# Kernel optimization log

Hardware: AMD Instinct MI355X
Metric: run time of the kernel (lower is better)

Reference implementation:

```python
import jax, jax.numpy as jnp
import numpy as np

EPS = 1e-7
MIN_NORM = 1e-15
PROJ_EPS = 1e-5
NEG_SLOPE = 0.2
HEADS = 4


def artanh(x):
    return jnp.arctanh(jnp.clip(x, -1.0 + EPS, 1.0 - EPS))


def _norm(x):
    return jnp.clip(jnp.linalg.norm(x, axis=-1, keepdims=True), MIN_NORM)


def proj(x):
    # project onto Poincare ball (c=1)
    n = _norm(x)
    maxn = 1.0 - PROJ_EPS
    return jnp.where(n > maxn, x / n * maxn, x)


def expmap0(u):
    n = _norm(u)
    return jnp.tanh(n) * u / n


def logmap0(x):
    n = _norm(x)
    return artanh(n) * x / n


def mobius_add(x, y):
    x2 = jnp.sum(x * x, axis=-1, keepdims=True)
    y2 = jnp.sum(y * y, axis=-1, keepdims=True)
    xy = jnp.sum(x * y, axis=-1, keepdims=True)
    num = (1.0 + 2.0 * xy + y2) * x + (1.0 - x2) * y
    den = 1.0 + 2.0 * xy + x2 * y2
    return num / jnp.clip(den, MIN_NORM)


def pdist(x, y):
    # Poincare distance, c=1 -> [...,] scalar
    ma = mobius_add(-x, y)
    return 2.0 * artanh(jnp.linalg.norm(ma, axis=-1))


def mobius_scalar_mul(r, x):
    n = _norm(x)
    return jnp.tanh(r * artanh(n)) * x / n


def mobius_matvec(W, x):
    # x: [N,din], W: [dout,din]
    mx = x @ W.T
    n_x = _norm(x)
    n_mx = _norm(mx)
    return jnp.tanh(n_mx / n_x * artanh(n_x)) * mx / n_mx


def segment_softmax(logits, seg, num_segments):
    m = jax.ops.segment_max(logits, seg, num_segments=num_segments)
    m = jnp.where(jnp.isfinite(m), m, 0.0)
    e = jnp.exp(logits - m[seg])
    s = jax.ops.segment_sum(e, seg, num_segments=num_segments)
    return e / (s[seg] + 1e-16)


def setup_inputs() -> dict:
    N, E, D = 50000, 500000, 128
    H = HEADS
    Dh = D // H
    ks = jax.random.split(jax.random.key(0), 12)
    # edges without self-loops (reference re-adds them, mirroring remove/add_self_loops)
    src = jax.random.randint(ks[0], (E,), 0, N)
    off = jax.random.randint(ks[1], (E,), 1, N)
    dst = (src + off) % N
    edge_index = jnp.stack([src, dst]).astype(jnp.int32)
    x_e = 0.1 * jax.random.normal(ks[2], (N, D), dtype=jnp.float32)
    x_h = proj(expmap0(0.05 * jax.random.normal(ks[3], (N, D), dtype=jnp.float32)))
    sc = 1.0 / np.sqrt(D)
    W_e = sc * jax.random.normal(ks[4], (D, D), dtype=jnp.float32)
    b_lin_e = jnp.zeros((D,), jnp.float32)
    att_e = 0.1 * jax.random.normal(ks[5], (1, H, 2 * Dh), dtype=jnp.float32)
    b_e = jnp.zeros((D,), jnp.float32)
    W_h = sc * jax.random.normal(ks[6], (D, D), dtype=jnp.float32)
    b_lin_h = jnp.zeros((D,), jnp.float32)
    att_h = 0.1 * jax.random.normal(ks[7], (1, H, 2 * Dh), dtype=jnp.float32)
    b_h = jnp.zeros((D,), jnp.float32)
    att_hf = 0.1 * jax.random.normal(ks[8], (1, 1), dtype=jnp.float32)
    att_ef = 0.1 * jax.random.normal(ks[9], (1, 1), dtype=jnp.float32)
    return {"x_e": x_e, "x_h": x_h, "edge_index": edge_index,
            "W_e": W_e, "b_lin_e": b_lin_e, "att_e": att_e, "b_e": b_e,
            "W_h": W_h, "b_lin_h": b_lin_h, "att_h": att_h, "b_h": b_h,
            "att_hf": att_hf, "att_ef": att_ef}


def reference(x_e, x_h, edge_index, W_e, b_lin_e, att_e, b_e,
              W_h, b_lin_h, att_h, b_h, att_hf, att_ef):
    N, D = x_e.shape
    H = HEADS
    Dh = att_e.shape[-1] // 2
    loop = jnp.arange(N, dtype=edge_index.dtype)
    src = jnp.concatenate([edge_index[0], loop])  # j (source)
    dst = jnp.concatenate([edge_index[1], loop])  # i (target, softmax segment)

    # ---- Euclidean GAT branch (GATConv) ----
    xe = (x_e @ W_e.T + b_lin_e).reshape(N, H, Dh)
    a_i = jnp.sum(xe * att_e[:, :, :Dh], axis=-1)  # [N,H] target part
    a_j = jnp.sum(xe * att_e[:, :, Dh:], axis=-1)  # [N,H] source part
    alpha = jax.nn.leaky_relu(a_i[dst] + a_j[src], NEG_SLOPE)  # [E',H]
    alpha = segment_softmax(alpha, dst, N)
    agg = jax.ops.segment_sum(xe[src] * alpha[:, :, None], dst, num_segments=N)
    e_out = jax.nn.relu(agg.reshape(N, H * Dh) + b_e)

    # ---- Hyperbolic GAT branch (HGATConv with HypLinear) ----
    mv = proj(mobius_matvec(W_h, x_h))
    hb = proj(expmap0(b_lin_h))  # proj_tan0 is identity on Poincare ball
    xh = proj(mobius_add(mv, hb))  # [N,D] hyperbolic points (original_x)
    lx = logmap0(xh).reshape(N, H, Dh)
    hi = jnp.sum(lx * att_h[:, :, :Dh], axis=-1)
    hj = jnp.sum(lx * att_h[:, :, Dh:], axis=-1)
    alpha_h = hi[dst] + hj[src]  # [E',H]
    d = pdist(xh[dst], xh[src])  # [E'] hyperbolic edge distances
    d = segment_softmax(d, dst, N)[:, None]
    alpha_h = jax.nn.leaky_relu(alpha_h * d, NEG_SLOPE)
    alpha_h = segment_softmax(alpha_h, dst, N)
    agg_h = jax.ops.segment_sum(lx[src] * alpha_h[:, :, None], dst, num_segments=N)
    out_t = jax.nn.relu(agg_h.reshape(N, H * Dh) + b_h)  # tangent at origin
    h_out = proj(expmap0(out_t))

    # ---- HFusion: fuse Euclidean into hyperbolic ----
    ye = proj(expmap0(e_out))
    dist_f = (pdist(h_out, ye) * att_hf[0, 0])[:, None]  # [N,1]
    xe2 = proj(mobius_scalar_mul(dist_f, ye))
    h_fused = proj(mobius_add(h_out, xe2))

    # ---- EFusion: fuse hyperbolic into Euclidean ----
    lh = logmap0(h_out)
    de = (jnp.sum((lh - e_out) ** 2, axis=-1) * att_ef[0, 0])[:, None]
    e_fused = e_out + de * lh

    return jnp.stack([h_fused, e_fused])  # [2,N,D]
```

## Files before the change

### kernel.cpp

```cpp
#include <hip/hip_runtime.h>
#include <hip/hip_fp16.h>
#include <math.h>

typedef _Float16 h2 __attribute__((ext_vector_type(2)));
typedef _Float16 h8 __attribute__((ext_vector_type(8)));
typedef float f32x4 __attribute__((ext_vector_type(4)));

#define MAXN_BALL (1.0f - 1e-5f)
#define ART_CLIP  (1.0f - 1e-7f)
#define MAXD 48
#define SROW 64

__device__ __forceinline__ float f_rcp(float x)  { return __builtin_amdgcn_rcpf(x); }
__device__ __forceinline__ float f_exp(float x)  { return __expf(x); }
__device__ __forceinline__ float f_log(float x)  { return __logf(x); }
__device__ __forceinline__ float f_tanh(float x) {
    float ax = fabsf(x);
    float e = __expf(2.f * ax);
    float t = 1.f - 2.f * f_rcp(e + 1.f);
    return copysignf(t, x);
}
__device__ __forceinline__ float f_atanh(float x) {
    x = fminf(x, ART_CLIP);
    return 0.5f * f_log((1.f + x) * f_rcp(1.f - x));
}
__device__ __forceinline__ float leaky(float x) { return x > 0.0f ? x : 0.2f * x; }

union F4H8 { float4 f; h2 h[4]; };
union F2H4 { float2 f; h2 h[2]; };
union H8U  { h8 v; h2 h[4]; };
union H8F  { float4 f; h8 v; h2 h[4]; };

__device__ __forceinline__ h2 pk16(float x, float y) {
    union { decltype(__builtin_amdgcn_cvt_pkrtz(0.f, 0.f)) a; h2 b; } u;
    u.a = __builtin_amdgcn_cvt_pkrtz(x, y);
    return u.b;
}

__global__ __launch_bounds__(256) void k_wcvt(const float* __restrict__ W0,
                                              const float* __restrict__ W1,
                                              h2* __restrict__ W16,
                                              int* __restrict__ slots,
                                              int N, int cblocks) {
    int b = blockIdx.x, t = threadIdx.x;
    if (b < cblocks) {
        int zi = b * 256 + t;
        if (zi < N) slots[zi * SROW] = 0;
        return;
    }
    int tw = (b - cblocks) * 256 + t;
    const float* W = (tw < 2048) ? W0 : W1;
    int c = (tw & 2047) * 8;
    float4 a = *(const float4*)(W + c);
    float4 bb = *(const float4*)(W + c + 4);
    F4H8 u;
    u.h[0] = pk16(a.x, a.y);  u.h[1] = pk16(a.z, a.w);
    u.h[2] = pk16(bb.x, bb.y); u.h[3] = pk16(bb.z, bb.w);
    *(float4*)&W16[(tw >> 11) * 8192 + (c >> 1)] = u.f;
}

__global__ __launch_bounds__(256) void k_prep_fused(
        const float* __restrict__ x_e, const float* __restrict__ x_h,
        const h2* __restrict__ W16,
        const float* __restrict__ b_lin_e, const float* __restrict__ b_lin_h,
        const float* __restrict__ att_e, const float* __restrict__ att_h,
        h2* __restrict__ xe16, h2* __restrict__ xh16,
        float* __restrict__ aux_j, float* __restrict__ aux_i,
        const int* __restrict__ ei, int* __restrict__ slots,
        int N, int E) {
    int t = threadIdx.x;
    if (blockIdx.y == 1) {
        int idx = blockIdx.x * 256 + t;
        if (idx < E + N) {
            int s, d;
            if (idx < E) { s = ei[idx]; d = ei[E + idx]; } else { s = d = idx - E; }
            int p = atomicAdd(&slots[d * SROW], 1);
            if (p < MAXD) slots[d * SROW + 1 + p] = s;
        }
        return;
    }
    int wv = t >> 6, l = t & 63;
    int rt = blockIdx.x * 4 + wv;
    if (rt * 16 >= N) return;
    int lane16 = l & 15, quad = l >> 4;
    int r = rt * 16 + lane16;
    int rr = (r < N) ? r : (N - 1);

    const float* Xrow = &x_e[(size_t)rr * 128 + quad * 8];
    H8U bfr[4];
#pragma unroll
    for (int ks = 0; ks < 4; ++ks) {
        float4 xa = *(const float4*)(Xrow + ks * 32);
        float4 xb = *(const float4*)(Xrow + ks * 32 + 4);
        bfr[ks].h[0] = pk16(xa.x, xa.y); bfr[ks].h[1] = pk16(xa.z, xa.w);
        bfr[ks].h[2] = pk16(xb.x, xb.y); bfr[ks].h[3] = pk16(xb.z, xb.w);
    }
    float pi[4] = {0.f, 0.f, 0.f, 0.f}, pj[4] = {0.f, 0.f, 0.f, 0.f};
#pragma unroll
    for (int ct = 0; ct < 8; ++ct) {
        const h2* Wrow = &W16[(ct * 16 + lane16) * 64 + quad * 4];
        f32x4 acc = {0.f, 0.f, 0.f, 0.f};
#pragma unroll
        for (int ks = 0; ks < 4; ++ks) {
            H8F a;
            a.f = *(const float4*)(Wrow + ks * 16);
            acc = __builtin_amdgcn_mfma_f32_16x16x32_f16(a.v, bfr[ks].v, acc, 0, 0, 0);
        }
        int obase = ct * 16 + quad * 4;
        float4 bb = *(const float4*)&b_lin_e[obase];
        F2H4 u;
        u.h[0] = pk16(acc[0] + bb.x, acc[1] + bb.y);
        u.h[1] = pk16(acc[2] + bb.z, acc[3] + bb.w);
        if (r < N) *(float2*)&xe16[(size_t)r * 64 + (obase >> 1)] = u.f;
        float4 xe4 = make_float4((float)u.h[0].x, (float)u.h[0].y,
                                 (float)u.h[1].x, (float)u.h[1].y);
        int hd = ct >> 1, w0 = (ct & 1) * 16 + quad * 4;
        float4 aT = *(const float4*)&att_e[hd * 64 + w0];
        float4 aS = *(const float4*)&att_e[hd * 64 + 32 + w0];
        pi[hd] += xe4.x * aT.x + xe4.y * aT.y + xe4.z * aT.z + xe4.w * aT.w;
        pj[hd] += xe4.x * aS.x + xe4.y * aS.y + xe4.z * aS.z + xe4.w * aS.w;
    }

    const float* Xrow1 = &x_h[(size_t)rr * 128 + quad * 8];
    float nx2 = 0.f;
#pragma unroll
    for (int ks = 0; ks < 4; ++ks) {
        float4 xa = *(const float4*)(Xrow1 + ks * 32);
        float4 xb = *(const float4*)(Xrow1 + ks * 32 + 4);
        nx2 += xa.x * xa.x + xa.y * xa.y + xa.z * xa.z + xa.w * xa.w
             + xb.x * xb.x + xb.y * xb.y + xb.z * xb.z + xb.w * xb.w;
        bfr[ks].h[0] = pk16(xa.x, xa.y); bfr[ks].h[1] = pk16(xa.z, xa.w);
        bfr[ks].h[2] = pk16(xb.x, xb.y); bfr[ks].h[3] = pk16(xb.z, xb.w);
    }
    f32x4 mx[8];
    float4 bh[8];
    float nmx2 = 0.f, dmb = 0.f, nb2 = 0.f;
#pragma unroll
    for (int ct = 0; ct < 8; ++ct) {
        const h2* Wrow = &W16[8192 + (ct * 16 + lane16) * 64 + quad * 4];
        f32x4 acc = {0.f, 0.f, 0.f, 0.f};
#pragma unroll
        for (int ks = 0; ks < 4; ++ks) {
            H8F a;
            a.f = *(const float4*)(Wrow + ks * 16);
            acc = __builtin_amdgcn_mfma_f32_16x16x32_f16(a.v, bfr[ks].v, acc, 0, 0, 0);
        }
        mx[ct] = acc;
        int obase = ct * 16 + quad * 4;
        float4 bv = *(const float4*)&b_lin_h[obase];
        bh[ct] = bv;
        nmx2 += acc[0] * acc[0] + acc[1] * acc[1] + acc[2] * acc[2] + acc[3] * acc[3];
        dmb  += acc[0] * bv.x + acc[1] * bv.y + acc[2] * bv.z + acc[3] * bv.w;
        nb2  += bv.x * bv.x + bv.y * bv.y + bv.z * bv.z + bv.w * bv.w;
    }
#pragma unroll
    for (int m = 16; m <= 32; m <<= 1) {
        nx2 += __shfl_xor(nx2, m, 64); nmx2 += __shfl_xor(nmx2, m, 64);
        dmb += __shfl_xor(dmb, m, 64); nb2  += __shfl_xor(nb2, m, 64);
    }

    float nxr = sqrtf(nx2),  nxc = fmaxf(nxr, 1e-15f);
    float nmxr = sqrtf(nmx2), nmxc = fmaxf(nmxr, 1e-15f);
    float tt = f_tanh(nmxc * f_rcp(nxc) * f_atanh(nxc));
    float c_m = tt * f_rcp(nmxc);
    float nmv = tt * (nmxr * f_rcp(nmxc));
    if (nmv > MAXN_BALL) { c_m *= MAXN_BALL / nmv; nmv = MAXN_BALL; }

    float nbr = sqrtf(nb2), nbc = fmaxf(nbr, 1e-15f);
    float tb = f_tanh(nbc);
    float c_b = tb * f_rcp(nbc);
    float nhb = tb * (nbr * f_rcp(nbc));
    if (nhb > MAXN_BALL) { c_b *= MAXN_BALL / nhb; nhb = MAXN_BALL; }

    float xy = c_m * c_b * dmb;
    float x2 = nmv * nmv, y2 = nhb * nhb;
    float den = fmaxf(1.f + 2.f * xy + x2 * y2, 1e-15f);
    float rden = f_rcp(den);
    float al = (1.f + 2.f * xy + y2) * c_m * rden;
    float be = (1.f - x2) * c_b * rden;
    float nr2 = al * al * nmx2 + 2.f * al * be * dmb + be * be * nb2;
    float nrr = sqrtf(nr2);
    if (nrr > MAXN_BALL) { float sc = MAXN_BALL / nrr; al *= sc; be *= sc; }

    float nr2r = 0.f;
    float sT[4] = {0.f, 0.f, 0.f, 0.f}, sS[4] = {0.f, 0.f, 0.f, 0.f};
#pragma unroll
    for (int ct = 0; ct < 8; ++ct) {
        float4 resv;
        resv.x = al * mx[ct][0] + be * bh[ct].x;
        resv.y = al * mx[ct][1] + be * bh[ct].y;
        resv.z = al * mx[ct][2] + be * bh[ct].z;
        resv.w = al * mx[ct][3] + be * bh[ct].w;
        F2H4 u;
        u.h[0] = pk16(resv.x, resv.y);
        u.h[1] = pk16(resv.z, resv.w);
        int obase = ct * 16 + quad * 4;
        if (r < N) *(float2*)&xh16[(size_t)r * 64 + (obase >> 1)] = u.f;
        float4 rv = make_float4((float)u.h[0].x, (float)u.h[0].y,
                                (float)u.h[1].x, (float)u.h[1].y);
        nr2r += rv.x * rv.x + rv.y * rv.y + rv.z * rv.z + rv.w * rv.w;
        int hd = ct >> 1, w0 = (ct & 1) * 16 + quad * 4;
        float4 hT = *(const float4*)&att_h[hd * 64 + w0];
        float4 hS = *(const float4*)&att_h[hd * 64 + 32 + w0];
        sT[hd] += rv.x * hT.x + rv.y * hT.y + rv.z * hT.z + rv.w * hT.w;
        sS[hd] += rv.x * hS.x + rv.y * hS.y + rv.z * hS.z + rv.w * hS.w;
    }
#pragma unroll
    for (int m = 16; m <= 32; m <<= 1) {
        nr2r += __shfl_xor(nr2r, m, 64);
#pragma unroll
        for (int hd = 0; hd < 4; ++hd) {
            pi[hd] += __shfl_xor(pi[hd], m, 64);
            pj[hd] += __shfl_xor(pj[hd], m, 64);
            sT[hd] += __shfl_xor(sT[hd], m, 64);
            sS[hd] += __shfl_xor(sS[hd], m, 64);
        }
    }
    float nrrr = sqrtf(nr2r);
    float nnc = fmaxf(nrrr, 1e-15f);
    float lam = f_atanh(nnc) * f_rcp(nnc);

    if (quad == 0 && r < N) {
        float4 qj4 = make_float4(lam * sS[0], lam * sS[1], lam * sS[2], lam * sS[3]);
        float4 pj4 = make_float4(pj[0], pj[1], pj[2], pj[3]);
        *(float4*)&aux_j[(size_t)r * 16]     = qj4;
        *(float4*)&aux_j[(size_t)r * 16 + 4] = pj4;
        *(float2*)&aux_j[(size_t)r * 16 + 8] = make_float2(lam, nr2r);
        float4 qi4 = make_float4(lam * sT[0], lam * sT[1], lam * sT[2], lam * sT[3]);
        float4 pi4 = make_float4(pi[0], pi[1], pi[2], pi[3]);
        *(float4*)&aux_i[(size_t)r * 8]     = qi4;
        *(float4*)&aux_i[(size_t)r * 8 + 4] = pi4;
    }
}

__global__ __launch_bounds__(256) void k_node_final(
    const h2* __restrict__ xh16, const float* __restrict__ aux_j,
    const float* __restrict__ aux_i, const h2* __restrict__ xe16,
    const int* __restrict__ slots,
    const float* __restrict__ b_e, const float* __restrict__ b_h,
    const float* __restrict__ att_hf, const float* __restrict__ att_ef,
    float* __restrict__ out, int N) {
    __shared__ int   s_src_all[8][MAXD];
    __shared__ float s_d_all[8][MAXD];
    __shared__ float s_ah_all[8][MAXD * 4];
    __shared__ float s_ae_all[8][MAXD * 4];

    int t = threadIdx.x;
    int sl = t & 31, ni = t >> 5;
    int i = blockIdx.x * 8 + ni;
    if (i >= N) return;
    int*   s_src = s_src_all[ni];
    float* s_d   = s_d_all[ni];
    float* s_ah  = s_ah_all[ni];
    float* s_ae  = s_ae_all[ni];

    const int* srow = &slots[(uint32_t)i * SROW];
    int deg = srow[0];
    if (deg > MAXD) deg = MAXD;
    if (sl < deg)      s_src[sl]      = srow[1 + sl];
    if (sl + 32 < deg) s_src[sl + 32] = srow[33 + sl];

    float x2i = aux_j[(uint32_t)i * 16u + 9u];
    {
        int g = sl & 7, sub = sl >> 3;
        uint32_t goff = (uint32_t)(g * 8);
        const h2* xi = &xh16[(uint32_t)i * 64u + goff];
        F4H8 us0, us1;
        us0.f = *(const float4*)xi;
        us1.f = *(const float4*)(xi + 4);
        for (int p = 0; p * 4 < deg; ++p) {
            int e = p * 4 + sub;
            bool act = e < deg;
            float dot = 0.f;
            int j = 0;
            if (act) {
                j = s_src[e];
                uint32_t oj = (uint32_t)j * 64u + goff;
                F4H8 ua, ub;
                ua.f = *(const float4*)&xh16[oj];
                ub.f = *(const float4*)&xh16[oj + 4u];
#pragma unroll
                for (int k = 0; k < 4; ++k) dot = __builtin_amdgcn_fdot2(ua.h[k], us0.h[k], dot, false);
#pragma unroll
                for (int k = 0; k < 4; ++k) dot = __builtin_amdgcn_fdot2(ub.h[k], us1.h[k], dot, false);
            }
            dot += __shfl_xor(dot, 1, 64);
            dot += __shfl_xor(dot, 2, 64);
            dot += __shfl_xor(dot, 4, 64);
            if (act && g == 0) {
                float y2 = aux_j[(uint32_t)j * 16u + 9u];
                float xy = dot;
                float A = 1.f - 2.f * xy + y2;
                float B = 1.f - x2i;
                float den = fmaxf(1.f - 2.f * xy + x2i * y2, 1e-15f);
                float num2 = fmaxf(A * A * x2i - 2.f * A * B * xy + B * B * y2, 0.f);
                float nma = fminf(sqrtf(num2) * f_rcp(den), ART_CLIP);
                s_d[e] = f_log((1.f + nma) * f_rcp(1.f - nma));
            }
        }
    }

    float eA = (sl < deg)      ? f_exp(s_d[sl])      : 0.f;
    float eB = (sl + 32 < deg) ? f_exp(s_d[sl + 32]) : 0.f;
    float ssum = eA + eB;
#pragma unroll
    for (int m = 16; m >= 1; m >>= 1) ssum += __shfl_xor(ssum, m, 64);
    float dinv = f_rcp(ssum + 1e-16f);

    float4 hi4 = *(const float4*)&aux_i[(uint32_t)i * 8u];
    float4 ai4 = *(const float4*)&aux_i[(uint32_t)i * 8u + 4u];
    float4 vh_s[2], ve_s[2];
    float lam_s[2] = {0.f, 0.f};
    float4 sh = make_float4(0.f, 0.f, 0.f, 0.f), se = sh;
#pragma unroll
    for (int s = 0; s < 2; ++s) {
        int e = sl + 32 * s;
        if (e < deg) {
            int j = s_src[e];
            float ds = (s ? eB : eA) * dinv;
            uint32_t oj = (uint32_t)j * 16u;
            float4 hj4 = *(const float4*)&aux_j[oj];
            float4 aj4 = *(const float4*)&aux_j[oj + 4u];
            lam_s[s] = aux_j[oj + 8u];
            float4 vh, ve;
            vh.x = f_exp(leaky((hi4.x + hj4.x) * ds));
            vh.y = f_exp(leaky((hi4.y + hj4.y) * ds));
            vh.z = f_exp(leaky((hi4.z + hj4.z) * ds));
            vh.w = f_exp(leaky((hi4.w + hj4.w) * ds));
            ve.x = f_exp(leaky(ai4.x + aj4.x));
            ve.y = f_exp(leaky(ai4.y + aj4.y));
            ve.z = f_exp(leaky(ai4.z + aj4.z));
            ve.w = f_exp(leaky(ai4.w + aj4.w));
            vh_s[s] = vh; ve_s[s] = ve;
            sh.x += vh.x; sh.y += vh.y; sh.z += vh.z; sh.w += vh.w;
            se.x += ve.x; se.y += ve.y; se.z += ve.z; se.w += ve.w;
        }
    }
#pragma unroll
    for (int m = 16; m >= 1; m >>= 1) {
        sh.x += __shfl_xor(sh.x, m, 64); sh.y += __shfl_xor(sh.y, m, 64);
        sh.z += __shfl_xor(sh.z, m, 64); sh.w += __shfl_xor(sh.w, m, 64);
        se.x += __shfl_xor(se.x, m, 64); se.y += __shfl_xor(se.y, m, 64);
        se.z += __shfl_xor(se.z, m, 64); se.w += __shfl_xor(se.w, m, 64);
    }
    float4 rh = make_float4(f_rcp(sh.x + 1e-16f), f_rcp(sh.y + 1e-16f),
                            f_rcp(sh.z + 1e-16f), f_rcp(sh.w + 1e-16f));
    float4 re = make_float4(f_rcp(se.x + 1e-16f), f_rcp(se.y + 1e-16f),
                            f_rcp(se.z + 1e-16f), f_rcp(se.w + 1e-16f));
#pragma unroll
    for (int s = 0; s < 2; ++s) {
        int e = sl + 32 * s;
        if (e < deg) {
            float lamj = lam_s[s];
            float4 vh = vh_s[s], ve = ve_s[s];
            vh.x *= rh.x * lamj; vh.y *= rh.y * lamj; vh.z *= rh.z * lamj; vh.w *= rh.w * lamj;
            ve.x *= re.x; ve.y *= re.y; ve.z *= re.z; ve.w *= re.w;
            *(float4*)&s_ah[e * 4] = vh;
            *(float4*)&s_ae[e * 4] = ve;
        }
    }

    int hq = sl >> 3;
    uint32_t dsl = 2u * (uint32_t)sl;
    float4 aE = make_float4(0.f, 0.f, 0.f, 0.f), aH = aE;
    int e = 0;
    for (; e + 3 < deg; e += 4) {
        int j0 = s_src[e], j1 = s_src[e + 1], j2 = s_src[e + 2], j3 = s_src[e + 3];
        uint32_t o0 = (uint32_t)j0 * 64u + dsl, o1 = (uint32_t)j1 * 64u + dsl;
        uint32_t o2 = (uint32_t)j2 * 64u + dsl, o3 = (uint32_t)j3 * 64u + dsl;
        F2H4 ux0, uh0, ux1, uh1, ux2, uh2, ux3, uh3;
        ux0.f = *(const float2*)&xe16[o0]; uh0.f = *(const float2*)&xh16[o0];
        ux1.f = *(const float2*)&xe16[o1]; uh1.f = *(const float2*)&xh16[o1];
        ux2.f = *(const float2*)&xe16[o2]; uh2.f = *(const float2*)&xh16[o2];
        ux3.f = *(const float2*)&xe16[o3]; uh3.f = *(const float2*)&xh16[o3];
        float we0 = s_ae[e * 4 + hq],       wh0 = s_ah[e * 4 + hq];
        float we1 = s_ae[(e + 1) * 4 + hq], wh1 = s_ah[(e + 1) * 4 + hq];
        float we2 = s_ae[(e + 2) * 4 + hq], wh2 = s_ah[(e + 2) * 4 + hq];
        float we3 = s_ae[(e + 3) * 4 + hq], wh3 = s_ah[(e + 3) * 4 + hq];
        aE.x += we0 * (float)ux0.h[0].x + we1 * (float)ux1.h[0].x;
        aE.y += we0 * (float)ux0.h[0].y + we1 * (float)ux1.h[0].y;
        aE.z += we0 * (float)ux0.h[1].x + we1 * (float)ux1.h[1].x;
        aE.w += we0 * (float)ux0.h[1].y + we1 * (float)ux1.h[1].y;
        aH.x += wh0 * (float)uh0.h[0].x + wh1 * (float)uh1.h[0].x;
        aH.y += wh0 * (float)uh0.h[0].y + wh1 * (float)uh1.h[0].y;
        aH.z += wh0 * (float)uh0.h[1].x + wh1 * (float)uh1.h[1].x;
        aH.w += wh0 * (float)uh0.h[1].y + wh1 * (float)uh1.h[1].y;
        aE.x += we2 * (float)ux2.h[0].x + we3 * (float)ux3.h[0].x;
        aE.y += we2 * (float)ux2.h[0].y + we3 * (float)ux3.h[0].y;
        aE.z += we2 * (float)ux2.h[1].x + we3 * (float)ux3.h[1].x;
        aE.w += we2 * (float)ux2.h[1].y + we3 * (float)ux3.h[1].y;
        aH.x += wh2 * (float)uh2.h[0].x + wh3 * (float)uh3.h[0].x;
        aH.y += wh2 * (float)uh2.h[0].y + wh3 * (float)uh3.h[0].y;
        aH.z += wh2 * (float)uh2.h[1].x + wh3 * (float)uh3.h[1].x;
        aH.w += wh2 * (float)uh2.h[1].y + wh3 * (float)uh3.h[1].y;
    }
    for (; e + 1 < deg; e += 2) {
        int j0 = s_src[e], j1 = s_src[e + 1];
        uint32_t o0 = (uint32_t)j0 * 64u + dsl, o1 = (uint32_t)j1 * 64u + dsl;
        F2H4 ux0, uh0, ux1, uh1;
        ux0.f = *(const float2*)&xe16[o0]; uh0.f = *(const float2*)&xh16[o0];
        ux1.f = *(const float2*)&xe16[o1]; uh1.f = *(const float2*)&xh16[o1];
        float we0 = s_ae[e * 4 + hq], wh0 = s_ah[e * 4 + hq];
        float we1 = s_ae[(e + 1) * 4 + hq], wh1 = s_ah[(e + 1) * 4 + hq];
        aE.x += we0 * (float)ux0.h[0].x + we1 * (float)ux1.h[0].x;
        aE.y += we0 * (float)ux0.h[0].y + we1 * (float)ux1.h[0].y;
        aE.z += we0 * (float)ux0.h[1].x + we1 * (float)ux1.h[1].x;
        aE.w += we0 * (float)ux0.h[1].y + we1 * (float)ux1.h[1].y;
        aH.x += wh0 * (float)uh0.h[0].x + wh1 * (float)uh1.h[0].x;
        aH.y += wh0 * (float)uh0.h[0].y + wh1 * (float)uh1.h[0].y;
        aH.z += wh0 * (float)uh0.h[1].x + wh1 * (float)uh1.h[1].x;
        aH.w += wh0 * (float)uh0.h[1].y + wh1 * (float)uh1.h[1].y;
    }
    if (e < deg) {
        int j = s_src[e];
        uint32_t oj = (uint32_t)j * 64u + dsl;
        F2H4 ux, uh;
        ux.f = *(const float2*)&xe16[oj];
        uh.f = *(const float2*)&xh16[oj];
        float we = s_ae[e * 4 + hq], wh = s_ah[e * 4 + hq];
        aE.x += we * (float)ux.h[0].x; aE.y += we * (float)ux.h[0].y;
        aE.z += we * (float)ux.h[1].x; aE.w += we * (float)ux.h[1].y;
        aH.x += wh * (float)uh.h[0].x; aH.y += wh * (float)uh.h[0].y;
        aH.z += wh * (float)uh.h[1].x; aH.w += wh * (float)uh.h[1].y;
    }

    float4 be4 = *(const float4*)&b_e[4 * sl];
    float4 bh4 = *(const float4*)&b_h[4 * sl];
    float4 eo, ot;
    eo.x = fmaxf(aE.x + be4.x, 0.f); eo.y = fmaxf(aE.y + be4.y, 0.f);
    eo.z = fmaxf(aE.z + be4.z, 0.f); eo.w = fmaxf(aE.w + be4.w, 0.f);
    ot.x = fmaxf(aH.x + bh4.x, 0.f); ot.y = fmaxf(aH.y + bh4.y, 0.f);
    ot.z = fmaxf(aH.z + bh4.z, 0.f); ot.w = fmaxf(aH.w + bh4.w, 0.f);
    float n2  = ot.x * ot.x + ot.y * ot.y + ot.z * ot.z + ot.w * ot.w;
    float ne2 = eo.x * eo.x + eo.y * eo.y + eo.z * eo.z + eo.w * eo.w;
    float dot3 = ot.x * eo.x + ot.y * eo.y + ot.z * eo.z + ot.w * eo.w;
#pragma unroll
    for (int m = 16; m >= 1; m >>= 1) {
        n2 += __shfl_xor(n2, m, 64); ne2 += __shfl_xor(ne2, m, 64); dot3 += __shfl_xor(dot3, m, 64);
    }

    float n_raw = sqrtf(n2), n_c = fmaxf(n_raw, 1e-15f);
    float th = f_tanh(n_c);
    float c_h = th * f_rcp(n_c);
    float nh = th * (n_raw * f_rcp(n_c));
    if (nh > MAXN_BALL) { c_h *= MAXN_BALL / nh; nh = MAXN_BALL; }

    float nE_raw = sqrtf(ne2), nE_c = fmaxf(nE_raw, 1e-15f);
    float tE = f_tanh(nE_c);
    float c_e = tE * f_rcp(nE_c);
    float ny = tE * (nE_raw * f_rcp(nE_c));
    if (ny > MAXN_BALL) { c_e *= MAXN_BALL / ny; ny = MAXN_BALL; }

    float xyv = c_h * c_e * dot3;
    float x2f = nh * nh, y2f = ny * ny;
    float A = 1.f - 2.f * xyv + y2f, B = 1.f - x2f;
    float den = fmaxf(1.f - 2.f * xyv + x2f * y2f, 1e-15f);
    float num2 = fmaxf(A * A * x2f - 2.f * A * B * xyv + B * B * y2f, 0.f);
    float nma = fminf(sqrtf(num2) * f_rcp(den), ART_CLIP);
    float distf = f_log((1.f + nma) * f_rcp(1.f - nma)) * att_hf[0];
    float nyc = fmaxf(ny, 1e-15f);
    float s1 = f_tanh(distf * f_atanh(nyc)) * f_rcp(nyc);
    float nxe2 = fabsf(s1) * ny;
    if (nxe2 > MAXN_BALL) { s1 *= MAXN_BALL / nxe2; nxe2 = MAXN_BALL; }
    float xy2 = s1 * xyv;
    float y22 = nxe2 * nxe2;
    float rden2 = f_rcp(fmaxf(1.f + 2.f * xy2 + x2f * y22, 1e-15f));
    float alpha = (1.f + 2.f * xy2 + y22) * rden2 * c_h;
    float beta  = (1.f - x2f) * s1 * rden2 * c_e;
    float nf2 = alpha * alpha * n2 + 2.f * alpha * beta * dot3 + beta * beta * ne2;
    float nf = sqrtf(nf2);
    if (nf > MAXN_BALL) { float sc = MAXN_BALL / nf; alpha *= sc; beta *= sc; }

    float nhc = fmaxf(nh, 1e-15f);
    float gam = f_atanh(nhc) * f_rcp(nhc) * c_h;
    float de2 = gam * gam * n2 - 2.f * gam * dot3 + ne2;
    float dg = de2 * att_ef[0] * gam;

    float4 o1;
    o1.x = alpha * ot.x + beta * eo.x; o1.y = alpha * ot.y + beta * eo.y;
    o1.z = alpha * ot.z + beta * eo.z; o1.w = alpha * ot.w + beta * eo.w;
    *(float4*)&out[(size_t)i * 128 + 4 * sl] = o1;
    float4 o2;
    o2.x = eo.x + dg * ot.x; o2.y = eo.y + dg * ot.y;
    o2.z = eo.z + dg * ot.z; o2.w = eo.w + dg * ot.w;
    *(float4*)&out[(size_t)N * 128 + (size_t)i * 128 + 4 * sl] = o2;
}

extern "C" void kernel_launch(void* const* d_in, const int* in_sizes, int n_in,
                              void* d_out, int out_size, void* d_ws, size_t ws_size,
                              hipStream_t stream) {
    const float* x_e      = (const float*)d_in[0];
    const float* x_h      = (const float*)d_in[1];
    const int*   ei       = (const int*)d_in[2];
    const float* W_e      = (const float*)d_in[3];
    const float* b_lin_e  = (const float*)d_in[4];
    const float* att_e    = (const float*)d_in[5];
    const float* b_e      = (const float*)d_in[6];
    const float* W_h      = (const float*)d_in[7];
    const float* b_lin_h  = (const float*)d_in[8];
    const float* att_h    = (const float*)d_in[9];
    const float* b_h      = (const float*)d_in[10];
    const float* att_hf   = (const float*)d_in[11];
    const float* att_ef   = (const float*)d_in[12];

    int N = in_sizes[0] / 128;
    int E = in_sizes[2] / 2;
    int EN = E + N;

    char* ws = (char*)d_ws;
    size_t off = 0;
    auto alloc = [&](size_t bytes) -> void* {
        void* p = ws + off;
        off = (off + bytes + 255) & ~(size_t)255;
        return p;
    };
    h2*    W16   = (h2*)alloc((size_t)2 * 8192 * 4);
    h2*    xe16  = (h2*)alloc((size_t)N * 128 * 2);
    h2*    xh16  = (h2*)alloc((size_t)N * 128 * 2);
    float* aux_j = (float*)alloc((size_t)N * 16 * 4);
    float* aux_i = (float*)alloc((size_t)N * 8 * 4);
    int*   slots = (int*)alloc((size_t)N * SROW * 4);

    int cblocks = (N + 255) / 256;
    k_wcvt<<<cblocks + 16, 256, 0, stream>>>(W_e, W_h, W16, slots, N, cblocks);

    int rtiles = (N + 15) / 16;
    int rblocks = (rtiles + 3) / 4;
    int eblocks = (EN + 255) / 256;
    int gx = rblocks > eblocks ? rblocks : eblocks;
    dim3 pgrid(gx, 2);
    k_prep_fused<<<pgrid, 256, 0, stream>>>(x_e, x_h, W16, b_lin_e, b_lin_h,
                                            att_e, att_h, xe16, xh16, aux_j, aux_i,
                                            ei, slots, N, E);

    int fblocks = (N + 7) / 8;
    k_node_final<<<fblocks, 256, 0, stream>>>(xh16, aux_j, aux_i, xe16,
                                              slots, b_e, b_h, att_hf, att_ef,
                                              (float*)d_out, N);
}
```

Baseline: 255.8 us.

## Interleave edge-slot scatter with node GEMM work in the same threads

Instead of a 2D grid where half the blocks do edge bucketing and half do the node MFMA transform, every block now first issues atomics for up to three edges per thread, then performs the node GEMM/hyperbolic prep, and only afterwards writes the source index into the reserved slot. This hides atomic latency behind the matrix work and halves the block count. The bias reload in the final loop also replaces keeping bh in registers, lowering register pressure. It risks fewer blocks in flight, and a leftover loop handles edges beyond three per thread.

Measured after the change: 261.5 us. 2.3% more time.

```diff
diff --git a/kernel.cpp b/kernel.cpp
--- a/kernel.cpp
+++ b/kernel.cpp
@@ -69,167 +69,188 @@
         const int* __restrict__ ei, int* __restrict__ slots,
         int N, int E) {
     int t = threadIdx.x;
-    if (blockIdx.y == 1) {
-        int idx = blockIdx.x * 256 + t;
-        if (idx < E + N) {
+    int bx = blockIdx.x;
+    int tid = bx * 256 + t;
+    int TOT = (int)gridDim.x * 256;
+    int EN = E + N;
+
+    int es[3], ed[3], ep[3];
+    bool ea[3];
+#pragma unroll
+    for (int k = 0; k < 3; ++k) {
+        int idx = tid + k * TOT;
+        ea[k] = idx < EN;
+        es[k] = 0; ed[k] = 0; ep[k] = MAXD;
+        if (ea[k]) {
             int s, d;
             if (idx < E) { s = ei[idx]; d = ei[E + idx]; } else { s = d = idx - E; }
-            int p = atomicAdd(&slots[d * SROW], 1);
-            if (p < MAXD) slots[d * SROW + 1 + p] = s;
-        }
-        return;
-    }
+            es[k] = s; ed[k] = d;
+            ep[k] = atomicAdd(&slots[d * SROW], 1);
+        }
+    }
+    for (int idx = tid + 3 * TOT; idx < EN; idx += TOT) {
+        int s, d;
+        if (idx < E) { s = ei[idx]; d = ei[E + idx]; } else { s = d = idx - E; }
+        int p = atomicAdd(&slots[d * SROW], 1);
+        if (p < MAXD) slots[d * SROW + 1 + p] = s;
+    }
+
     int wv = t >> 6, l = t & 63;
-    int rt = blockIdx.x * 4 + wv;
-    if (rt * 16 >= N) return;
-    int lane16 = l & 15, quad = l >> 4;
-    int r = rt * 16 + lane16;
-    int rr = (r < N) ? r : (N - 1);
-
-    const float* Xrow = &x_e[(size_t)rr * 128 + quad * 8];
-    H8U bfr[4];
-#pragma unroll
-    for (int ks = 0; ks < 4; ++ks) {
-        float4 xa = *(const float4*)(Xrow + ks * 32);
-        float4 xb = *(const float4*)(Xrow + ks * 32 + 4);
-        bfr[ks].h[0] = pk16(xa.x, xa.y); bfr[ks].h[1] = pk16(xa.z, xa.w);
-        bfr[ks].h[2] = pk16(xb.x, xb.y); bfr[ks].h[3] = pk16(xb.z, xb.w);
-    }
-    float pi[4] = {0.f, 0.f, 0.f, 0.f}, pj[4] = {0.f, 0.f, 0.f, 0.f};
-#pragma unroll
-    for (int ct = 0; ct < 8; ++ct) {
-        const h2* Wrow = &W16[(ct * 16 + lane16) * 64 + quad * 4];
-        f32x4 acc = {0.f, 0.f, 0.f, 0.f};
+    int rt = bx * 4 + wv;
+    if (rt * 16 < N) {
+        int lane16 = l & 15, quad = l >> 4;
+        int r = rt * 16 + lane16;
+        int rr = (r < N) ? r : (N - 1);
+
+        const float* Xrow = &x_e[(size_t)rr * 128 + quad * 8];
+        H8U bfr[4];
 #pragma unroll
         for (int ks = 0; ks < 4; ++ks) {
-            H8F a;
-            a.f = *(const float4*)(Wrow + ks * 16);
-            acc = __builtin_amdgcn_mfma_f32_16x16x32_f16(a.v, bfr[ks].v, acc, 0, 0, 0);
-        }
-        int obase = ct * 16 + quad * 4;
-        float4 bb = *(const float4*)&b_lin_e[obase];
-        F2H4 u;
-        u.h[0] = pk16(acc[0] + bb.x, acc[1] + bb.y);
-        u.h[1] = pk16(acc[2] + bb.z, acc[3] + bb.w);
-        if (r < N) *(float2*)&xe16[(size_t)r * 64 + (obase >> 1)] = u.f;
-        float4 xe4 = make_float4((float)u.h[0].x, (float)u.h[0].y,
-                                 (float)u.h[1].x, (float)u.h[1].y);
-        int hd = ct >> 1, w0 = (ct & 1) * 16 + quad * 4;
-        float4 aT = *(const float4*)&att_e[hd * 64 + w0];
-        float4 aS = *(const float4*)&att_e[hd * 64 + 32 + w0];
-        pi[hd] += xe4.x * aT.x + xe4.y * aT.y + xe4.z * aT.z + xe4.w * aT.w;
-        pj[hd] += xe4.x * aS.x + xe4.y * aS.y + xe4.z * aS.z + xe4.w * aS.w;
-    }
-
-    const float* Xrow1 = &x_h[(size_t)rr * 128 + quad * 8];
-    float nx2 = 0.f;
-#pragma unroll
-    for (int ks = 0; ks < 4; ++ks) {
-        float4 xa = *(const float4*)(Xrow1 + ks * 32);
-        float4 xb = *(const float4*)(Xrow1 + ks * 32 + 4);
-        nx2 += xa.x * xa.x + xa.y * xa.y + xa.z * xa.z + xa.w * xa.w
-             + xb.x * xb.x + xb.y * xb.y + xb.z * xb.z + xb.w * xb.w;
-        bfr[ks].h[0] = pk16(xa.x, xa.y); bfr[ks].h[1] = pk16(xa.z, xa.w);
-        bfr[ks].h[2] = pk16(xb.x, xb.y); bfr[ks].h[3] = pk16(xb.z, xb.w);
-    }
-    f32x4 mx[8];
-    float4 bh[8];
-    float nmx2 = 0.f, dmb = 0.f, nb2 = 0.f;
-#pragma unroll
-    for (int ct = 0; ct < 8; ++ct) {
-        const h2* Wrow = &W16[8192 + (ct * 16 + lane16) * 64 + quad * 4];
-        f32x4 acc = {0.f, 0.f, 0.f, 0.f};
+            float4 xa = *(const float4*)(Xrow + ks * 32);
+            float4 xb = *(const float4*)(Xrow + ks * 32 + 4);
+            bfr[ks].h[0] = pk16(xa.x, xa.y); bfr[ks].h[1] = pk16(xa.z, xa.w);
+            bfr[ks].h[2] = pk16(xb.x, xb.y); bfr[ks].h[3] = pk16(xb.z, xb.w);
+        }
+        float pi[4] = {0.f, 0.f, 0.f, 0.f}, pj[4] = {0.f, 0.f, 0.f, 0.f};
+#pragma unroll
+        for (int ct = 0; ct < 8; ++ct) {
+            const h2* Wrow = &W16[(ct * 16 + lane16) * 64 + quad * 4];
+            f32x4 acc = {0.f, 0.f, 0.f, 0.f};
+#pragma unroll
+            for (int ks = 0; ks < 4; ++ks) {
+                H8F a;
+                a.f = *(const float4*)(Wrow + ks * 16);
+                acc = __builtin_amdgcn_mfma_f32_16x16x32_f16(a.v, bfr[ks].v, acc, 0, 0, 0);
+            }
+            int obase = ct * 16 + quad * 4;
+            float4 bb = *(const float4*)&b_lin_e[obase];
+            F2H4 u;
+            u.h[0] = pk16(acc[0] + bb.x, acc[1] + bb.y);
+            u.h[1] = pk16(acc[2] + bb.z, acc[3] + bb.w);
+            if (r < N) *(float2*)&xe16[(size_t)r * 64 + (obase >> 1)] = u.f;
+            float4 xe4 = make_float4((float)u.h[0].x, (float)u.h[0].y,
+                                     (float)u.h[1].x, (float)u.h[1].y);
+            int hd = ct >> 1, w0 = (ct & 1) * 16 + quad * 4;
+            float4 aT = *(const float4*)&att_e[hd * 64 + w0];
+            float4 aS = *(const float4*)&att_e[hd * 64 + 32 + w0];
+            pi[hd] += xe4.x * aT.x + xe4.y * aT.y + xe4.z * aT.z + xe4.w * aT.w;
+            pj[hd] += xe4.x * aS.x + xe4.y * aS.y + xe4.z * aS.z + xe4.w * aS.w;
+        }
+
+        const float* Xrow1 = &x_h[(size_t)rr * 128 + quad * 8];
+        float nx2 = 0.f;
 #pragma unroll
         for (int ks = 0; ks < 4; ++ks) {
-            H8F a;
-            a.f = *(const float4*)(Wrow + ks * 16);
-            acc = __builtin_amdgcn_mfma_f32_16x16x32_f16(a.v, bfr[ks].v, acc, 0, 0, 0);
-        }
-        mx[ct] = acc;
-        int obase = ct * 16 + quad * 4;
-        float4 bv = *(const float4*)&b_lin_h[obase];
-        bh[ct] = bv;
-        nmx2 += acc[0] * acc[0] + acc[1] * acc[1] + acc[2] * acc[2] + acc[3] * acc[3];
-        dmb  += acc[0] * bv.x + acc[1] * bv.y + acc[2] * bv.z + acc[3] * bv.w;
-        nb2  += bv.x * bv.x + bv.y * bv.y + bv.z * bv.z + bv.w * bv.w;
-    }
-#pragma unroll
-    for (int m = 16; m <= 32; m <<= 1) {
-        nx2 += __shfl_xor(nx2, m, 64); nmx2 += __shfl_xor(nmx2, m, 64);
-        dmb += __shfl_xor(dmb, m, 64); nb2  += __shfl_xor(nb2, m, 64);
-    }
-
-    float nxr = sqrtf(nx2),  nxc = fmaxf(nxr, 1e-15f);
-    float nmxr = sqrtf(nmx2), nmxc = fmaxf(nmxr, 1e-15f);
-    float tt = f_tanh(nmxc * f_rcp(nxc) * f_atanh(nxc));
-    float c_m = tt * f_rcp(nmxc);
-    float nmv = tt * (nmxr * f_rcp(nmxc));
-    if (nmv > MAXN_BALL) { c_m *= MAXN_BALL / nmv; nmv = MAXN_BALL; }
-
-    float nbr = sqrtf(nb2), nbc = fmaxf(nbr, 1e-15f);
-    float tb = f_tanh(nbc);
-    float c_b = tb * f_rcp(nbc);
-    float nhb = tb * (nbr * f_rcp(nbc));
-    if (nhb > MAXN_BALL) { c_b *= MAXN_BALL / nhb; nhb = MAXN_BALL; }
-
-    float xy = c_m * c_b * dmb;
-    float x2 = nmv * nmv, y2 = nhb * nhb;
-    float den = fmaxf(1.f + 2.f * xy + x2 * y2, 1e-15f);
-    float rden = f_rcp(den);
-    float al = (1.f + 2.f * xy + y2) * c_m * rden;
-    float be = (1.f - x2) * c_b * rden;
-    float nr2 = al * al * nmx2 + 2.f * al * be * dmb + be * be * nb2;
-    float nrr = sqrtf(nr2);
-    if (nrr > MAXN_BALL) { float sc = MAXN_BALL / nrr; al *= sc; be *= sc; }
-
-    float nr2r = 0.f;
-    float sT[4] = {0.f, 0.f, 0.f, 0.f}, sS[4] = {0.f, 0.f, 0.f, 0.f};
-#pragma unroll
-    for (int ct = 0; ct < 8; ++ct) {
-        float4 resv;
-        resv.x = al * mx[ct][0] + be * bh[ct].x;
-        resv.y = al * mx[ct][1] + be * bh[ct].y;
-        resv.z = al * mx[ct][2] + be * bh[ct].z;
-        resv.w = al * mx[ct][3] + be * bh[ct].w;
-        F2H4 u;
-        u.h[0] = pk16(resv.x, resv.y);
-        u.h[1] = pk16(resv.z, resv.w);
-        int obase = ct * 16 + quad * 4;
-        if (r < N) *(float2*)&xh16[(size_t)r * 64 + (obase >> 1)] = u.f;
-        float4 rv = make_float4((float)u.h[0].x, (float)u.h[0].y,
-                                (float)u.h[1].x, (float)u.h[1].y);
-        nr2r += rv.x * rv.x + rv.y * rv.y + rv.z * rv.z + rv.w * rv.w;
-        int hd = ct >> 1, w0 = (ct & 1) * 16 + quad * 4;
-        float4 hT = *(const float4*)&att_h[hd * 64 + w0];
-        float4 hS = *(const float4*)&att_h[hd * 64 + 32 + w0];
-        sT[hd] += rv.x * hT.x + rv.y * hT.y + rv.z * hT.z + rv.w * hT.w;
-        sS[hd] += rv.x * hS.x + rv.y * hS.y + rv.z * hS.z + rv.w * hS.w;
-    }
-#pragma unroll
-    for (int m = 16; m <= 32; m <<= 1) {
-        nr2r += __shfl_xor(nr2r, m, 64);
-#pragma unroll
-        for (int hd = 0; hd < 4; ++hd) {
-            pi[hd] += __shfl_xor(pi[hd], m, 64);
-            pj[hd] += __shfl_xor(pj[hd], m, 64);
-            sT[hd] += __shfl_xor(sT[hd], m, 64);
-            sS[hd] += __shfl_xor(sS[hd], m, 64);
-        }
-    }
-    float nrrr = sqrtf(nr2r);
-    float nnc = fmaxf(nrrr, 1e-15f);
-    float lam = f_atanh(nnc) * f_rcp(nnc);
-
-    if (quad == 0 && r < N) {
-        float4 qj4 = make_float4(lam * sS[0], lam * sS[1], lam * sS[2], lam * sS[3]);
-        float4 pj4 = make_float4(pj[0], pj[1], pj[2], pj[3]);
-        *(float4*)&aux_j[(size_t)r * 16]     = qj4;
-        *(float4*)&aux_j[(size_t)r * 16 + 4] = pj4;
-        *(float2*)&aux_j[(size_t)r * 16 + 8] = make_float2(lam, nr2r);
-        float4 qi4 = make_float4(lam * sT[0], lam * sT[1], lam * sT[2], lam * sT[3]);
-        float4 pi4 = make_float4(pi[0], pi[1], pi[2], pi[3]);
-        *(float4*)&aux_i[(size_t)r * 8]     = qi4;
-        *(float4*)&aux_i[(size_t)r * 8 + 4] = pi4;
+            float4 xa = *(const float4*)(Xrow1 + ks * 32);
+            float4 xb = *(const float4*)(Xrow1 + ks * 32 + 4);
+            nx2 += xa.x * xa.x + xa.y * xa.y + xa.z * xa.z + xa.w * xa.w
+                 + xb.x * xb.x + xb.y * xb.y + xb.z * xb.z + xb.w * xb.w;
+            bfr[ks].h[0] = pk16(xa.x, xa.y); bfr[ks].h[1] = pk16(xa.z, xa.w);
+            bfr[ks].h[2] = pk16(xb.x, xb.y); bfr[ks].h[3] = pk16(xb.z, xb.w);
+        }
+        f32x4 mx[8];
+        float nmx2 = 0.f, dmb = 0.f, nb2 = 0.f;
+#pragma unroll
+        for (int ct = 0; ct < 8; ++ct) {
+            const h2* Wrow = &W16[8192 + (ct * 16 + lane16) * 64 + quad * 4];
+            f32x4 acc = {0.f, 0.f, 0.f, 0.f};
+#pragma unroll
+            for (int ks = 0; ks < 4; ++ks) {
+                H8F a;
+                a.f = *(const float4*)(Wrow + ks * 16);
+                acc = __builtin_amdgcn_mfma_f32_16x16x32_f16(a.v, bfr[ks].v, acc, 0, 0, 0);
+            }
+            mx[ct] = acc;
+            int obase = ct * 16 + quad * 4;
+            float4 bv = *(const float4*)&b_lin_h[obase];
+            nmx2 += acc[0] * acc[0] + acc[1] * acc[1] + acc[2] * acc[2] + acc[3] * acc[3];
+            dmb  += acc[0] * bv.x + acc[1] * bv.y + acc[2] * bv.z + acc[3] * bv.w;
+            nb2  += bv.x * bv.x + bv.y * bv.y + bv.z * bv.z + bv.w * bv.w;
+        }
+#pragma unroll
+        for (int m = 16; m <= 32; m <<= 1) {
+            nx2 += __shfl_xor(nx2, m, 64); nmx2 += __shfl_xor(nmx2, m, 64);
+            dmb += __shfl_xor(dmb, m, 64); nb2  += __shfl_xor(nb2, m, 64);
+        }
+
+        float nxr = sqrtf(nx2),  nxc = fmaxf(nxr, 1e-15f);
+        float nmxr = sqrtf(nmx2), nmxc = fmaxf(nmxr, 1e-15f);
+        float tt = f_tanh(nmxc * f_rcp(nxc) * f_atanh(nxc));
+        float c_m = tt * f_rcp(nmxc);
+        float nmv = tt * (nmxr * f_rcp(nmxc));
+        if (nmv > MAXN_BALL) { c_m *= MAXN_BALL / nmv; nmv = MAXN_BALL; }
+
+        float nbr = sqrtf(nb2), nbc = fmaxf(nbr, 1e-15f);
+        float tb = f_tanh(nbc);
+        float c_b = tb * f_rcp(nbc);
+        float nhb = tb * (nbr * f_rcp(nbc));
+        if (nhb > MAXN_BALL) { c_b *= MAXN_BALL / nhb; nhb = MAXN_BALL; }
+
+        float xy = c_m * c_b * dmb;
+        float x2 = nmv * nmv, y2 = nhb * nhb;
+        float den = fmaxf(1.f + 2.f * xy + x2 * y2, 1e-15f);
+        float rden = f_rcp(den);
+        float al = (1.f + 2.f * xy + y2) * c_m * rden;
+        float be = (1.f - x2) * c_b * rden;
+        float nr2 = al * al * nmx2 + 2.f * al * be * dmb + be * be * nb2;
+        float nrr = sqrtf(nr2);
+        if (nrr > MAXN_BALL) { float sc = MAXN_BALL / nrr; al *= sc; be *= sc; }
+
+        float nr2r = 0.f;
+        float sT[4] = {0.f, 0.f, 0.f, 0.f}, sS[4] = {0.f, 0.f, 0.f, 0.f};
+#pragma unroll
+        for (int ct = 0; ct < 8; ++ct) {
+            int obase = ct * 16 + quad * 4;
+            float4 bv = *(const float4*)&b_lin_h[obase];
+            float4 resv;
+            resv.x = al * mx[ct][0] + be * bv.x;
+            resv.y = al * mx[ct][1] + be * bv.y;
+            resv.z = al * mx[ct][2] + be * bv.z;
+            resv.w = al * mx[ct][3] + be * bv.w;
+            F2H4 u;
+            u.h[0] = pk16(resv.x, resv.y);
+            u.h[1] = pk16(resv.z, resv.w);
+            if (r < N) *(float2*)&xh16[(size_t)r * 64 + (obase >> 1)] = u.f;
+            float4 rv = make_float4((float)u.h[0].x, (float)u.h[0].y,
+                                    (float)u.h[1].x, (float)u.h[1].y);
+            nr2r += rv.x * rv.x + rv.y * rv.y + rv.z * rv.z + rv.w * rv.w;
+            int hd = ct >> 1, w0 = (ct & 1) * 16 + quad * 4;
+            float4 hT = *(const float4*)&att_h[hd * 64 + w0];
+            float4 hS = *(const float4*)&att_h[hd * 64 + 32 + w0];
+            sT[hd] += rv.x * hT.x + rv.y * hT.y + rv.z * hT.z + rv.w * hT.w;
+            sS[hd] += rv.x * hS.x + rv.y * hS.y + rv.z * hS.z + rv.w * hS.w;
+        }
+#pragma unroll
+        for (int m = 16; m <= 32; m <<= 1) {
+            nr2r += __shfl_xor(nr2r, m, 64);
+#pragma unroll
+            for (int hd = 0; hd < 4; ++hd) {
+                pi[hd] += __shfl_xor(pi[hd], m, 64);
+                pj[hd] += __shfl_xor(pj[hd], m, 64);
+                sT[hd] += __shfl_xor(sT[hd], m, 64);
+                sS[hd] += __shfl_xor(sS[hd], m, 64);
+            }
+        }
+        float nrrr = sqrtf(nr2r);
+        float nnc = fmaxf(nrrr, 1e-15f);
+        float lam = f_atanh(nnc) * f_rcp(nnc);
+
+        if (quad == 0 && r < N) {
+            float4 qj4 = make_float4(lam * sS[0], lam * sS[1], lam * sS[2], lam * sS[3]);
+            float4 pj4 = make_float4(pj[0], pj[1], pj[2], pj[3]);
+            *(float4*)&aux_j[(size_t)r * 16]     = qj4;
+            *(float4*)&aux_j[(size_t)r * 16 + 4] = pj4;
+            *(float2*)&aux_j[(size_t)r * 16 + 8] = make_float2(lam, nr2r);
+            float4 qi4 = make_float4(lam * sT[0], lam * sT[1], lam * sT[2], lam * sT[3]);
+            float4 pi4 = make_float4(pi[0], pi[1], pi[2], pi[3]);
+            *(float4*)&aux_i[(size_t)r * 8]     = qi4;
+            *(float4*)&aux_i[(size_t)r * 8 + 4] = pi4;
+        }
+    }
+
+#pragma unroll
+    for (int k = 0; k < 3; ++k) {
+        if (ea[k] && ep[k] < MAXD) slots[ed[k] * SROW + 1 + ep[k]] = es[k];
     }
 }
 
@@ -505,7 +526,6 @@
 
     int N = in_sizes[0] / 128;
     int E = in_sizes[2] / 2;
-    int EN = E + N;
 
     char* ws = (char*)d_ws;
     size_t off = 0;
@@ -526,12 +546,9 @@
 
     int rtiles = (N + 15) / 16;
     int rblocks = (rtiles + 3) / 4;
-    int eblocks = (EN + 255) / 256;
-    int gx = rblocks > eblocks ? rblocks : eblocks;
-    dim3 pgrid(gx, 2);
-    k_prep_fused<<<pgrid, 256, 0, stream>>>(x_e, x_h, W16, b_lin_e, b_lin_h,
-                                            att_e, att_h, xe16, xh16, aux_j, aux_i,
-                                            ei, slots, N, E);
+    k_prep_fused<<<rblocks, 256, 0, stream>>>(x_e, x_h, W16, b_lin_e, b_lin_h,
+                                              att_e, att_h, xe16, xh16, aux_j, aux_i,
+                                              ei, slots, N, E);
 
     int fblocks = (N + 7) / 8;
     k_node_final<<<fblocks, 256, 0, stream>>>(xh16, aux_j, aux_i, xe16,
```
